# Optimization experiments

Measured on AMD Instinct MI355X. Metric: run time of the kernel, lower is better.

Reference implementation:

```python
import jax, jax.numpy as jnp
import numpy as np

B, N, DIM, H, DH = 2, 2048, 1024, 16, 64
INNER = H * DH
ROPE_BASE = 10000.0


def setup_inputs() -> dict:
    key = jax.random.key(0)
    ks = jax.random.split(key, 6)
    s = 0.02
    return {
        "x": jax.random.normal(ks[0], (B, N, DIM), jnp.float32),
        "Wq": jax.random.normal(ks[1], (DIM, INNER), jnp.float32) * s,
        "Wk": jax.random.normal(ks[2], (DIM, INNER), jnp.float32) * s,
        "Wv": jax.random.normal(ks[3], (DIM, INNER), jnp.float32) * s,
        "Wo": jax.random.normal(ks[4], (INNER, DIM), jnp.float32) * s,
        "bo": jnp.zeros((DIM,), jnp.float32),
    }


def _rotate_half(x):
    # einops '... (d r) -> ... d r' with r=2: x1 = even lanes, x2 = odd lanes,
    # then cat((-x2, x1), dim=-1)
    x1 = x[..., 0::2]
    x2 = x[..., 1::2]
    return jnp.concatenate([-x2, x1], axis=-1)


def _rope_sin_cos(n, d, dtype):
    # inv_freq over arange(0, d, 2); emb = cat(f, f) -> length d
    inv_freq = 1.0 / (ROPE_BASE ** (jnp.arange(0, d, 2, dtype=jnp.float32) / d))
    f = jnp.arange(n, dtype=jnp.float32)[:, None] * inv_freq[None, :]  # [n, d/2]
    e = jnp.concatenate([f, f], axis=-1)  # [n, d]
    return jnp.sin(e).astype(dtype), jnp.cos(e).astype(dtype)


def _apply_rope(t, sin, cos):
    # t: [b, h, n, d]; sin/cos: [n, d]; rot_dim == d (full head), t_pass empty
    return t * cos[None, None] + _rotate_half(t) * sin[None, None]


def reference(x, Wq, Wk, Wv, Wo, bo):
    b, n, _ = x.shape
    scale = DH ** (-0.5)

    def split_heads(y):  # [b, n, h*d] -> [b, h, n, d]
        return y.reshape(b, n, H, DH).transpose(0, 2, 1, 3)

    q = split_heads(x @ Wq)
    k = split_heads(x @ Wk)
    v = split_heads(x @ Wv)

    sin, cos = _rope_sin_cos(n, DH, x.dtype)
    q = _apply_rope(q, sin, cos)
    k = _apply_rope(k, sin, cos)

    # causal SDPA (mask=None path -> is_causal=True), eval mode so dropout_p=0
    scores = jnp.einsum("bhqd,bhkd->bhqk", q, k) * scale
    causal = jnp.tril(jnp.ones((n, n), dtype=bool))
    scores = jnp.where(causal[None, None], scores, jnp.finfo(scores.dtype).min)
    probs = jax.nn.softmax(scores, axis=-1)
    attn = jnp.einsum("bhqk,bhkd->bhqd", probs, v)

    out = attn.transpose(0, 2, 1, 3).reshape(b, n, INNER) @ Wo + bo
    return out, k, v
```

## Files before the change

### kernel.cpp

```cpp
#include <hip/hip_runtime.h>
#include <cstdint>
#include <cmath>

#define BB   2
#define NN   2048
#define DIMM 1024
#define NHH  16
#define DHH  64
#define MMR  (BB * NN)

typedef _Float16 half8  __attribute__((ext_vector_type(8)));
typedef _Float16 half4v __attribute__((ext_vector_type(4)));
typedef float    f32x4  __attribute__((ext_vector_type(4)));

#define GLD16(gp, lp)                                                          \
  __builtin_amdgcn_global_load_lds(                                            \
      (const __attribute__((address_space(1))) unsigned int*)(gp),             \
      (__attribute__((address_space(3))) unsigned int*)(lp), 16, 0, 0)

__global__ __launch_bounds__(256) void cvt_x_kernel(const float* __restrict__ x,
                                                    _Float16* __restrict__ xh) {
  int i = (blockIdx.x * 256 + threadIdx.x) * 4;
  float4 v = *(const float4*)(x + i);
  half4v h;
  h[0] = (_Float16)v.x; h[1] = (_Float16)v.y;
  h[2] = (_Float16)v.z; h[3] = (_Float16)v.w;
  *(half4v*)(xh + i) = h;
}

__global__ __launch_bounds__(256) void transpose_w_kernel(
    const float* __restrict__ Wq, const float* __restrict__ Wk,
    const float* __restrict__ Wv, const float* __restrict__ Wo,
    _Float16* __restrict__ wt) {
  __shared__ float tile[64][65];
  int z = blockIdx.z;
  const float* W = (z == 0) ? Wq : (z == 1) ? Wk : (z == 2) ? Wv : Wo;
  _Float16* dst = wt + (size_t)z * 1024 * 1024;
  int r0 = blockIdx.x * 64;
  int c0 = blockIdx.y * 64;
  int t = threadIdx.x;
  int tr = t >> 4;
  int tc = (t & 15) * 4;
#pragma unroll
  for (int i = 0; i < 4; ++i) {
    float4 v = *(const float4*)(W + (size_t)(r0 + tr + i * 16) * 1024 + c0 + tc);
    tile[tr + i * 16][tc + 0] = v.x;
    tile[tr + i * 16][tc + 1] = v.y;
    tile[tr + i * 16][tc + 2] = v.z;
    tile[tr + i * 16][tc + 3] = v.w;
  }
  __syncthreads();
#pragma unroll
  for (int i = 0; i < 4; ++i) {
    int nl = tr + i * 16;
    half4v hv;
    hv[0] = (_Float16)tile[tc + 0][nl];
    hv[1] = (_Float16)tile[tc + 1][nl];
    hv[2] = (_Float16)tile[tc + 2][nl];
    hv[3] = (_Float16)tile[tc + 3][nl];
    *(half4v*)(dst + (size_t)(c0 + nl) * 1024 + r0 + tc) = hv;
  }
}

__global__ __launch_bounds__(256) void gemm_qkv_kernel(
    const _Float16* __restrict__ xh, const _Float16* __restrict__ wt,
    float* __restrict__ ko, float* __restrict__ vo,
    _Float16* __restrict__ qh, _Float16* __restrict__ kh,
    _Float16* __restrict__ vth) {
  __shared__ __align__(16) char smem[32768];
  _Float16* As = (_Float16*)smem;
  _Float16* Bs = (_Float16*)(smem + 16384);
  float (*Cs)[65] = (float(*)[65])smem;

  const int m0  = blockIdx.x * 64;
  const int ngl = blockIdx.y * 64;
  const int mat = ngl >> 10;
  const int n0  = ngl & 1023;
  const _Float16* wb = wt + (size_t)mat * 1024 * 1024;
  const int t = threadIdx.x;
  const int wv = t >> 6, lane = t & 63, l16 = lane & 15, quad = lane >> 4;
  const int r  = t >> 3;
  const int cl = t & 7;
  const int csw = (cl ^ (r & 7)) * 8;
  const _Float16* pa0 = xh + (size_t)(m0 + r) * 1024 + csw;
  const _Float16* pa1 = pa0 + 32 * 1024;
  const _Float16* pb0 = wb + (size_t)(n0 + r) * 1024 + csw;
  const _Float16* pb1 = pb0 + 32 * 1024;
  f32x4 acc[4] = {};
  const int arow = wv * 16 + l16;
  const int a7 = arow & 7;
  GLD16(pa0, As + wv * 512);
  GLD16(pa1, As + 2048 + wv * 512);
  GLD16(pb0, Bs + wv * 512);
  GLD16(pb1, Bs + 2048 + wv * 512);
  int cur = 0;
  for (int k0 = 0; k0 < 1024; k0 += 64) {
    if (k0 + 64 < 1024) {
      const int nb = cur ^ 1;
      GLD16(pa0 + k0 + 64, As + nb * 4096 + wv * 512);
      GLD16(pa1 + k0 + 64, As + nb * 4096 + 2048 + wv * 512);
      GLD16(pb0 + k0 + 64, Bs + nb * 4096 + wv * 512);
      GLD16(pb1 + k0 + 64, Bs + nb * 4096 + 2048 + wv * 512);
      asm volatile("s_waitcnt vmcnt(4)" ::: "memory");
    } else {
      asm volatile("s_waitcnt vmcnt(0)" ::: "memory");
    }
    __builtin_amdgcn_s_barrier();
    asm volatile("" ::: "memory");
    const _Float16* Ab = As + cur * 4096;
    const _Float16* Bb = Bs + cur * 4096;
    half8 af0 = *(const half8*)(Ab + arow * 64 + (quad ^ a7) * 8);
    half8 af1 = *(const half8*)(Ab + arow * 64 + ((4 + quad) ^ a7) * 8);
#pragma unroll
    for (int nt = 0; nt < 4; ++nt) {
      int brow = nt * 16 + l16;
      int b7 = brow & 7;
      half8 bf0 = *(const half8*)(Bb + brow * 64 + (quad ^ b7) * 8);
      half8 bf1 = *(const half8*)(Bb + brow * 64 + ((4 + quad) ^ b7) * 8);
      acc[nt] = __builtin_amdgcn_mfma_f32_16x16x32_f16(af0, bf0, acc[nt], 0, 0, 0);
      acc[nt] = __builtin_amdgcn_mfma_f32_16x16x32_f16(af1, bf1, acc[nt], 0, 0, 0);
    }
    asm volatile("s_waitcnt lgkmcnt(0)" ::: "memory");
    __builtin_amdgcn_s_barrier();
    asm volatile("" ::: "memory");
    cur ^= 1;
  }
#pragma unroll
  for (int nt = 0; nt < 4; ++nt)
#pragma unroll
    for (int rr = 0; rr < 4; ++rr)
      Cs[wv * 16 + quad * 4 + rr][nt * 16 + l16] = acc[nt][rr];
  __syncthreads();
  int lr = t >> 2;
  int cseg = (t & 3) * 16;
  int m = m0 + lr;
  int b = m >> 11;
  int pos = m & 2047;
  int h = n0 >> 6;
  int bhh = b * NHH + h;
  float vals[16];
  if (mat == 2) {
#pragma unroll
    for (int j = 0; j < 16; ++j) vals[j] = Cs[lr][cseg + j];
  } else {
    float fpos = (float)pos;
#pragma unroll
    for (int j = 0; j < 16; ++j) {
      int i = cseg + j;
      int jd = (i < 32) ? i : (i - 32);
      float invf = exp2f((float)jd * -0.41524101186092029f);
      float ang = fpos * invf;
      float sv, cv;
      sincosf(ang, &sv, &cv);
      float partner = (i < 32) ? -Cs[lr][2 * i + 1] : Cs[lr][2 * (i - 32)];
      vals[j] = Cs[lr][i] * cv + partner * sv;
    }
  }
  size_t rowb = ((size_t)bhh * NN + pos) * DHH + cseg;
  if (mat == 0) {
    half8 h0, h1;
#pragma unroll
    for (int j = 0; j < 8; ++j) { h0[j] = (_Float16)(vals[j] * 0.125f); h1[j] = (_Float16)(vals[8 + j] * 0.125f); }
    *(half8*)(qh + rowb) = h0;
    *(half8*)(qh + rowb + 8) = h1;
  } else if (mat == 1) {
#pragma unroll
    for (int j4 = 0; j4 < 4; ++j4) {
      float4 o;
      o.x = vals[j4 * 4 + 0]; o.y = vals[j4 * 4 + 1];
      o.z = vals[j4 * 4 + 2]; o.w = vals[j4 * 4 + 3];
      *(float4*)(ko + rowb + j4 * 4) = o;
    }
    half8 h0, h1;
#pragma unroll
    for (int j = 0; j < 8; ++j) { h0[j] = (_Float16)vals[j]; h1[j] = (_Float16)vals[8 + j]; }
    *(half8*)(kh + rowb) = h0;
    *(half8*)(kh + rowb + 8) = h1;
  } else {
#pragma unroll
    for (int j4 = 0; j4 < 4; ++j4) {
      float4 o;
      o.x = vals[j4 * 4 + 0]; o.y = vals[j4 * 4 + 1];
      o.z = vals[j4 * 4 + 2]; o.w = vals[j4 * 4 + 3];
      *(float4*)(vo + rowb + j4 * 4) = o;
    }
#pragma unroll
    for (int j = 0; j < 16; ++j)
      vth[((size_t)bhh * DHH + cseg + j) * NN + pos] = (_Float16)vals[j];
  }
}

__global__ __launch_bounds__(256, 2) void fattn_kernel(
    const _Float16* __restrict__ qh, const _Float16* __restrict__ kh,
    const _Float16* __restrict__ vth, _Float16* __restrict__ ah) {
  __shared__ __align__(16) _Float16 Kt[2][4096];
  __shared__ __align__(16) _Float16 Vt[2][4096];
  __shared__ __align__(16) _Float16 Pb[4][16][72];
  const int qb = 15 - (int)blockIdx.x;
  const int bh = blockIdx.y;
  const int t = threadIdx.x;
  const int wv = t >> 6, lane = t & 63, l16 = lane & 15, quad = lane >> 4;
  const int q0 = qb * 128;
  const _Float16* kg = kh + (size_t)bh * NN * DHH;
  const _Float16* vg = vth + (size_t)bh * DHH * NN;
  half8 qf[2][2];
#pragma unroll
  for (int qt2 = 0; qt2 < 2; ++qt2) {
    const _Float16* qp =
        qh + ((size_t)bh * NN + q0 + wv * 32 + qt2 * 16 + l16) * DHH + quad * 8;
    qf[qt2][0] = *(const half8*)qp;
    qf[qt2][1] = *(const half8*)(qp + 32);
  }
  half8 ones;
#pragma unroll
  for (int j = 0; j < 8; ++j) ones[j] = (_Float16)1.f;
  f32x4 o[2][4] = {};
  f32x4 ls[2] = {};
  const int ktmax = 2 * qb + 1;
#pragma unroll
  for (int iss = 0; iss < 2; ++iss) {
    int cid = iss * 256 + wv * 64 + lane;
    int row = cid >> 3;
    int c = (cid & 7) ^ (row & 7);
    GLD16(kg + (size_t)row * DHH + c * 8, &Kt[0][(iss * 256 + wv * 64) * 8]);
    GLD16(vg + (size_t)row * NN + c * 8, &Vt[0][(iss * 256 + wv * 64) * 8]);
  }
  int cur = 0;
  for (int kt = 0; kt <= ktmax; ++kt) {
    __syncthreads();
    if (kt < ktmax) {
      const _Float16* kn = kg + (size_t)(kt + 1) * 64 * DHH;
      const _Float16* vn = vg + (kt + 1) * 64;
      int nb = cur ^ 1;
#pragma unroll
      for (int iss = 0; iss < 2; ++iss) {
        int cid = iss * 256 + wv * 64 + lane;
        int row = cid >> 3;
        int c = (cid & 7) ^ (row & 7);
        GLD16(kn + (size_t)row * DHH + c * 8, &Kt[nb][(iss * 256 + wv * 64) * 8]);
        GLD16(vn + (size_t)row * NN + c * 8, &Vt[nb][(iss * 256 + wv * 64) * 8]);
      }
    }
    if (kt * 64 <= q0 + wv * 32 + 31) {
      half8 kf[4][2], vf[4][2];
      const _Float16* Kb = Kt[cur];
      const _Float16* Vb = Vt[cur];
#pragma unroll
      for (int nt = 0; nt < 4; ++nt) {
        int row = nt * 16 + l16;
        int r7 = row & 7;
        kf[nt][0] = *(const half8*)(Kb + row * 64 + ((quad ^ r7) * 8));
        kf[nt][1] = *(const half8*)(Kb + row * 64 + (((quad + 4) ^ r7) * 8));
        vf[nt][0] = *(const half8*)(Vb + row * 64 + ((quad ^ r7) * 8));
        vf[nt][1] = *(const half8*)(Vb + row * 64 + (((quad + 4) ^ r7) * 8));
      }
#pragma unroll
      for (int qt2 = 0; qt2 < 2; ++qt2) {
        int base = q0 + wv * 32 + qt2 * 16;
        if (kt * 64 <= base + 15) {
          f32x4 s4[4];
#pragma unroll
          for (int nt = 0; nt < 4; ++nt) {
            f32x4 z = {};
            z = __builtin_amdgcn_mfma_f32_16x16x32_f16(qf[qt2][0], kf[nt][0], z, 0, 0, 0);
            s4[nt] = __builtin_amdgcn_mfma_f32_16x16x32_f16(qf[qt2][1], kf[nt][1], z, 0, 0, 0);
          }
          if (kt * 64 + 63 > base) {
#pragma unroll
            for (int nt = 0; nt < 4; ++nt) {
              int key = kt * 64 + nt * 16 + l16;
#pragma unroll
              for (int r = 0; r < 4; ++r) {
                float p = (key > base + quad * 4 + r) ? 0.f : __expf(s4[nt][r]);
                Pb[wv][quad * 4 + r][nt * 16 + l16] = (_Float16)p;
              }
            }
          } else {
#pragma unroll
            for (int nt = 0; nt < 4; ++nt)
#pragma unroll
              for (int r = 0; r < 4; ++r)
                Pb[wv][quad * 4 + r][nt * 16 + l16] = (_Float16)__expf(s4[nt][r]);
          }
          asm volatile("s_waitcnt lgkmcnt(0)" ::: "memory");
          half8 pf0 = *(const half8*)&Pb[wv][l16][quad * 8];
          half8 pf1 = *(const half8*)&Pb[wv][l16][32 + quad * 8];
#pragma unroll
          for (int nt = 0; nt < 4; ++nt) {
            o[qt2][nt] = __builtin_amdgcn_mfma_f32_16x16x32_f16(pf0, vf[nt][0], o[qt2][nt], 0, 0, 0);
            o[qt2][nt] = __builtin_amdgcn_mfma_f32_16x16x32_f16(pf1, vf[nt][1], o[qt2][nt], 0, 0, 0);
          }
          ls[qt2] = __builtin_amdgcn_mfma_f32_16x16x32_f16(pf0, ones, ls[qt2], 0, 0, 0);
          ls[qt2] = __builtin_amdgcn_mfma_f32_16x16x32_f16(pf1, ones, ls[qt2], 0, 0, 0);
        }
      }
    }
    cur ^= 1;
  }
  const int b = bh >> 4, h = bh & 15;
#pragma unroll
  for (int qt2 = 0; qt2 < 2; ++qt2)
#pragma unroll
    for (int r = 0; r < 4; ++r) {
      float inv = 1.f / ls[qt2][r];
      int pos = q0 + wv * 32 + qt2 * 16 + quad * 4 + r;
      size_t ob = ((size_t)(b * NN + pos)) * DIMM + h * DHH;
#pragma unroll
      for (int nt = 0; nt < 4; ++nt)
        ah[ob + nt * 16 + l16] = (_Float16)(o[qt2][nt][r] * inv);
    }
}

__global__ __launch_bounds__(256) void gemm_out_kernel(
    const _Float16* __restrict__ ah, const _Float16* __restrict__ wot,
    const float* __restrict__ bo, float* __restrict__ out) {
  __shared__ __align__(16) char smem[32768];
  _Float16* As = (_Float16*)smem;
  _Float16* Bs = (_Float16*)(smem + 16384);
  const int m0 = blockIdx.x * 64;
  const int n0 = blockIdx.y * 64;
  const int t = threadIdx.x;
  const int wv = t >> 6, lane = t & 63, l16 = lane & 15, quad = lane >> 4;
  const int r  = t >> 3;
  const int cl = t & 7;
  const int csw = (cl ^ (r & 7)) * 8;
  const _Float16* pa0 = ah + (size_t)(m0 + r) * 1024 + csw;
  const _Float16* pa1 = pa0 + 32 * 1024;
  const _Float16* pb0 = wot + (size_t)(n0 + r) * 1024 + csw;
  const _Float16* pb1 = pb0 + 32 * 1024;
  f32x4 acc[4] = {};
  const int arow = wv * 16 + l16;
  const int a7 = arow & 7;
  GLD16(pa0, As + wv * 512);
  GLD16(pa1, As + 2048 + wv * 512);
  GLD16(pb0, Bs + wv * 512);
  GLD16(pb1, Bs + 2048 + wv * 512);
  int cur = 0;
  for (int k0 = 0; k0 < 1024; k0 += 64) {
    if (k0 + 64 < 1024) {
      const int nb = cur ^ 1;
      GLD16(pa0 + k0 + 64, As + nb * 4096 + wv * 512);
      GLD16(pa1 + k0 + 64, As + nb * 4096 + 2048 + wv * 512);
      GLD16(pb0 + k0 + 64, Bs + nb * 4096 + wv * 512);
      GLD16(pb1 + k0 + 64, Bs + nb * 4096 + 2048 + wv * 512);
      asm volatile("s_waitcnt vmcnt(4)" ::: "memory");
    } else {
      asm volatile("s_waitcnt vmcnt(0)" ::: "memory");
    }
    __builtin_amdgcn_s_barrier();
    asm volatile("" ::: "memory");
    const _Float16* Ab = As + cur * 4096;
    const _Float16* Bb = Bs + cur * 4096;
    half8 af0 = *(const half8*)(Ab + arow * 64 + (quad ^ a7) * 8);
    half8 af1 = *(const half8*)(Ab + arow * 64 + ((4 + quad) ^ a7) * 8);
#pragma unroll
    for (int nt = 0; nt < 4; ++nt) {
      int brow = nt * 16 + l16;
      int b7 = brow & 7;
      half8 bf0 = *(const half8*)(Bb + brow * 64 + (quad ^ b7) * 8);
      half8 bf1 = *(const half8*)(Bb + brow * 64 + ((4 + quad) ^ b7) * 8);
      acc[nt] = __builtin_amdgcn_mfma_f32_16x16x32_f16(af0, bf0, acc[nt], 0, 0, 0);
      acc[nt] = __builtin_amdgcn_mfma_f32_16x16x32_f16(af1, bf1, acc[nt], 0, 0, 0);
    }
    asm volatile("s_waitcnt lgkmcnt(0)" ::: "memory");
    __builtin_amdgcn_s_barrier();
    asm volatile("" ::: "memory");
    cur ^= 1;
  }
#pragma unroll
  for (int nt = 0; nt < 4; ++nt) {
    int col = n0 + nt * 16 + l16;
    float bias = bo[col];
#pragma unroll
    for (int rr = 0; rr < 4; ++rr) {
      out[(size_t)(m0 + wv * 16 + quad * 4 + rr) * 1024 + col] = acc[nt][rr] + bias;
    }
  }
}

extern "C" void kernel_launch(void* const* d_in, const int* in_sizes, int n_in,
                              void* d_out, int out_size, void* d_ws, size_t ws_size,
                              hipStream_t stream) {
  (void)in_sizes; (void)n_in; (void)out_size; (void)ws_size;
  const float* x  = (const float*)d_in[0];
  const float* Wq = (const float*)d_in[1];
  const float* Wk = (const float*)d_in[2];
  const float* Wv = (const float*)d_in[3];
  const float* Wo = (const float*)d_in[4];
  const float* bo = (const float*)d_in[5];

  float* out = (float*)d_out;
  float* ko  = out + (size_t)MMR * DIMM;
  float* vo  = ko + (size_t)BB * NHH * NN * DHH;

  char* w = (char*)d_ws;
  _Float16* xh  = (_Float16*)w;
  _Float16* ah  = (_Float16*)w;
  _Float16* wt  = (_Float16*)(w + (8u << 20));
  _Float16* qh  = (_Float16*)(w + (16u << 20));
  _Float16* kh  = (_Float16*)(w + (24u << 20));
  _Float16* vth = (_Float16*)(w + (32u << 20));

  hipLaunchKernelGGL(cvt_x_kernel, dim3(4096), dim3(256), 0, stream, x, xh);
  hipLaunchKernelGGL(transpose_w_kernel, dim3(16, 16, 4), dim3(256), 0, stream,
                     Wq, Wk, Wv, Wo, wt);
  hipLaunchKernelGGL(gemm_qkv_kernel, dim3(64, 48), dim3(256), 0, stream,
                     xh, wt, ko, vo, qh, kh, vth);
  hipLaunchKernelGGL(fattn_kernel, dim3(16, 32), dim3(256), 0, stream,
                     qh, kh, vth, ah);
  hipLaunchKernelGGL(gemm_out_kernel, dim3(64, 16), dim3(256), 0, stream,
                     ah, wt + (size_t)3 * 1024 * 1024, bo, out);
}
```

Before: 211.1 us.

## Triple-buffer K/V tiles in flash attention and remap blocks across XCDs

```diff
diff --git a/kernel.cpp b/kernel.cpp
--- a/kernel.cpp
+++ b/kernel.cpp
@@ -193,11 +193,14 @@
 __global__ __launch_bounds__(256, 2) void fattn_kernel(
     const _Float16* __restrict__ qh, const _Float16* __restrict__ kh,
     const _Float16* __restrict__ vth, _Float16* __restrict__ ah) {
-  __shared__ __align__(16) _Float16 Kt[2][4096];
-  __shared__ __align__(16) _Float16 Vt[2][4096];
+  __shared__ __align__(16) _Float16 Kt[3][4096];
+  __shared__ __align__(16) _Float16 Vt[3][4096];
   __shared__ __align__(16) _Float16 Pb[4][16][72];
-  const int qb = 15 - (int)blockIdx.x;
-  const int bh = blockIdx.y;
+  const int lin  = (int)blockIdx.x + 16 * (int)blockIdx.y;
+  const int xcd  = lin & 7;
+  const int slot = lin >> 3;
+  const int qb   = 15 - (slot & 15);
+  const int bh   = xcd * 4 + (slot >> 4);
   const int t = threadIdx.x;
   const int wv = t >> 6, lane = t & 63, l16 = lane & 15, quad = lane >> 4;
   const int q0 = qb * 128;
@@ -217,34 +220,41 @@
   f32x4 o[2][4] = {};
   f32x4 ls[2] = {};
   const int ktmax = 2 * qb + 1;
-#pragma unroll
-  for (int iss = 0; iss < 2; ++iss) {
-    int cid = iss * 256 + wv * 64 + lane;
-    int row = cid >> 3;
-    int c = (cid & 7) ^ (row & 7);
-    GLD16(kg + (size_t)row * DHH + c * 8, &Kt[0][(iss * 256 + wv * 64) * 8]);
-    GLD16(vg + (size_t)row * NN + c * 8, &Vt[0][(iss * 256 + wv * 64) * 8]);
-  }
+
+#define STAGE_KV(tile, nb) do {                                                \
+    const _Float16* kn_ = kg + (size_t)(tile) * 64 * DHH;                      \
+    const _Float16* vn_ = vg + (tile) * 64;                                    \
+    _Float16* kl_ = &Kt[nb][0];                                                \
+    _Float16* vl_ = &Vt[nb][0];                                                \
+    _Pragma("unroll")                                                          \
+    for (int iss = 0; iss < 2; ++iss) {                                        \
+      int cid = iss * 256 + wv * 64 + lane;                                    \
+      int row = cid >> 3;                                                      \
+      int c = (cid & 7) ^ (row & 7);                                           \
+      GLD16(kn_ + (size_t)row * DHH + c * 8, kl_ + (iss * 256 + wv * 64) * 8); \
+      GLD16(vn_ + (size_t)row * NN + c * 8, vl_ + (iss * 256 + wv * 64) * 8);  \
+    }                                                                          \
+  } while (0)
+
+  STAGE_KV(0, 0);
+  STAGE_KV(1, 1);
   int cur = 0;
   for (int kt = 0; kt <= ktmax; ++kt) {
-    __syncthreads();
-    if (kt < ktmax) {
-      const _Float16* kn = kg + (size_t)(kt + 1) * 64 * DHH;
-      const _Float16* vn = vg + (kt + 1) * 64;
-      int nb = cur ^ 1;
-#pragma unroll
-      for (int iss = 0; iss < 2; ++iss) {
-        int cid = iss * 256 + wv * 64 + lane;
-        int row = cid >> 3;
-        int c = (cid & 7) ^ (row & 7);
-        GLD16(kn + (size_t)row * DHH + c * 8, &Kt[nb][(iss * 256 + wv * 64) * 8]);
-        GLD16(vn + (size_t)row * NN + c * 8, &Vt[nb][(iss * 256 + wv * 64) * 8]);
-      }
-    }
+    if (kt + 2 <= ktmax) {
+      int nb = cur + 2; if (nb >= 3) nb -= 3;
+      STAGE_KV(kt + 2, nb);
+      asm volatile("s_waitcnt vmcnt(8)" ::: "memory");
+    } else if (kt + 1 <= ktmax) {
+      asm volatile("s_waitcnt vmcnt(4)" ::: "memory");
+    } else {
+      asm volatile("s_waitcnt vmcnt(0)" ::: "memory");
+    }
+    __builtin_amdgcn_s_barrier();
+    asm volatile("" ::: "memory");
     if (kt * 64 <= q0 + wv * 32 + 31) {
       half8 kf[4][2], vf[4][2];
-      const _Float16* Kb = Kt[cur];
-      const _Float16* Vb = Vt[cur];
+      const _Float16* Kb = &Kt[cur][0];
+      const _Float16* Vb = &Vt[cur][0];
 #pragma unroll
       for (int nt = 0; nt < 4; ++nt) {
         int row = nt * 16 + l16;
@@ -295,8 +305,12 @@
         }
       }
     }
-    cur ^= 1;
-  }
+    asm volatile("s_waitcnt lgkmcnt(0)" ::: "memory");
+    __builtin_amdgcn_s_barrier();
+    asm volatile("" ::: "memory");
+    cur = (cur == 2) ? 0 : cur + 1;
+  }
+#undef STAGE_KV
   const int b = bh >> 4, h = bh & 15;
 #pragma unroll
   for (int qt2 = 0; qt2 < 2; ++qt2)
```

After: 210.2 us. No clear change (-0.5%).
